# Kernel tuning notes

Measured on AMD Instinct MI355X. Metric: run time of the kernel, lower is better.

Reference implementation:

```python
import jax, jax.numpy as jnp
import numpy as np
import math

T, N, D, H = 1024, 8, 1024, 16
HD = D // H  # head_dim = 64


def setup_inputs() -> dict:
    key = jax.random.key(0)
    k1, k2, k3, k4 = jax.random.split(key, 4)
    scale = 1.0 / math.sqrt(D)  # roughly xavier-scale params
    return {
        "x": jax.random.normal(k1, (T, N, D), dtype=jnp.float32),
        "q_weight": jax.random.normal(k2, (D, H, HD), dtype=jnp.float32) * scale,
        "v_weight": jax.random.normal(k3, (D, H, HD), dtype=jnp.float32) * scale,
        "out_w": jax.random.normal(k4, (D, D), dtype=jnp.float32) * scale,
        "out_b": jnp.zeros((D,), dtype=jnp.float32),
    }


def reference(x, q_weight, v_weight, out_w, out_b):
    inv_sqrt_hd = 1.0 / math.sqrt(HD)
    # q = k : (T, N, H, HD)
    q = jnp.einsum('tbm,mhd->tbhd', x, q_weight)
    q_sq = jnp.einsum('tbhd,tbhd->tbh', q, q)  # squared norms
    # squared L2 distance logits: (T, S, N, H)
    squared_dist = q_sq[:, None] + q_sq[None, :] - 2.0 * jnp.einsum('tbhd,sbhd->tsbh', q, q)
    attn_logits = -squared_dist * inv_sqrt_hd
    attn_weights = jax.nn.softmax(attn_logits, axis=1)  # softmax over source dim S
    # A = W_q W_q^T per head: (H, D, D)
    A = jnp.einsum('mhd,nhd->hmn', q_weight, q_weight) * inv_sqrt_hd
    XA = jnp.einsum('tbm,hmn->tbhn', x, A)           # (T, N, H, D)
    PXA = jnp.einsum('tsbh,sbhm->tbhm', attn_weights, XA)  # (T, N, H, D)
    PXAV = jnp.einsum('tbhm,mhd->tbhd', PXA, v_weight).reshape(T, N, D)
    return PXAV @ out_w.T + out_b
```

## Files before the change

kernel.cpp:

```cpp
#include <hip/hip_runtime.h>
#include <hip/hip_bf16.h>

#define T_ 1024
#define N_ 8
#define D_ 1024
#define H_ 16
#define HD_ 64

typedef __attribute__((ext_vector_type(8))) short bf16x8;
typedef __attribute__((ext_vector_type(4))) float f32x4;
typedef __attribute__((ext_vector_type(16))) float f32x16;
typedef __attribute__((ext_vector_type(4))) int i32x4;
typedef __attribute__((ext_vector_type(2))) int i32x2;
typedef unsigned short u16;
typedef unsigned int u32;

__device__ __forceinline__ float bf2f(u16 u){
  union { float f; unsigned int i; } v; v.i = ((unsigned int)u) << 16; return v.f;
}
__device__ __forceinline__ u16 f2bf(float f){
  union { float f; unsigned int i; } v; v.f = f;
  unsigned int r = v.i + 0x7FFFu + ((v.i >> 16) & 1u);
  return (u16)(r >> 16);
}
__device__ __forceinline__ u16 f2bf_fast(float f){
  __hip_bfloat16 h = __float2bfloat16(f);
  return *reinterpret_cast<u16*>(&h);
}
__device__ __forceinline__ float exp2_raw(float x){
  float r;
  asm("v_exp_f32 %0, %1" : "=v"(r) : "v"(x));
  return r;
}
__device__ __forceinline__ void gl_lds16(const u16* g, u16* l){
  __builtin_amdgcn_global_load_lds(
      (const __attribute__((address_space(1))) unsigned int*)g,
      (__attribute__((address_space(3))) unsigned int*)(unsigned int)(unsigned long long)l,
      16, 0, 0);
}

__global__ __launch_bounds__(256) void k_wqt(const float* __restrict__ Wq, u16* __restrict__ Wqt){
  __shared__ float tld[64][65];
  int m0 = blockIdx.x * 64, n0 = blockIdx.y * 64;
  int col = threadIdx.x & 63, rq = threadIdx.x >> 6;
  #pragma unroll
  for (int p = 0; p < 16; ++p){
    int row = rq * 16 + p;
    tld[row][col] = Wq[(size_t)(m0 + row) * D_ + n0 + col];
  }
  __syncthreads();
  #pragma unroll
  for (int p = 0; p < 16; ++p){
    int row = rq * 16 + p;
    Wqt[(size_t)(n0 + row) * D_ + m0 + col] = f2bf(tld[col][row]);
  }
}

__global__ __launch_bounds__(256) void k_bmatp(const float* __restrict__ qw, const float* __restrict__ vw,
                                               float* __restrict__ Bp){
  int h = (int)blockIdx.x >> 3, sp = (int)blockIdx.x & 7;
  int tid = threadIdx.x, lane = tid & 63, w = tid >> 6;
  int g = lane >> 4, c = lane & 15;
  __shared__ u16 Qt[64 * 72];
  __shared__ u16 Vt[64 * 72];
  f32x4 zero = {0.f, 0.f, 0.f, 0.f};
  f32x4 acc[4];
  #pragma unroll
  for (int eb = 0; eb < 4; ++eb) acc[eb] = zero;
  int m = tid >> 2, cg = tid & 3;
  for (int mt = sp * 128; mt < sp * 128 + 128; mt += 64){
    __syncthreads();
    #pragma unroll
    for (int q = 0; q < 4; ++q){
      int e0 = cg * 16 + q * 4;
      f32x4 vq = *(const f32x4*)(qw + (size_t)(mt + m) * D_ + h * 64 + e0);
      f32x4 vv = *(const f32x4*)(vw + (size_t)(mt + m) * D_ + h * 64 + e0);
      #pragma unroll
      for (int j = 0; j < 4; ++j){
        Qt[(e0 + j) * 72 + m] = f2bf_fast(vq[j]);
        Vt[(e0 + j) * 72 + m] = f2bf_fast(vv[j]);
      }
    }
    __syncthreads();
    #pragma unroll
    for (int kk = 0; kk < 2; ++kk){
      bf16x8 av = *(const bf16x8*)&Vt[(w * 16 + c) * 72 + kk * 32 + g * 8];
      #pragma unroll
      for (int eb = 0; eb < 4; ++eb){
        bf16x8 bq = *(const bf16x8*)&Qt[(eb * 16 + c) * 72 + kk * 32 + g * 8];
        acc[eb] = __builtin_amdgcn_mfma_f32_16x16x32_bf16(av, bq, acc[eb], 0, 0, 0);
      }
    }
  }
  #pragma unroll
  for (int eb = 0; eb < 4; ++eb)
    #pragma unroll
    for (int r = 0; r < 4; ++r){
      int d = w * 16 + g * 4 + r, e = eb * 16 + c;
      Bp[(((size_t)sp * 16 + h) * 64 + d) * 64 + e] = acc[eb][r];
    }
}

__global__ __launch_bounds__(256) void k_bred(const float* __restrict__ Bp, u16* __restrict__ Bt){
  int i = blockIdx.x * 256 + threadIdx.x;
  float s = 0.f;
  #pragma unroll
  for (int j = 0; j < 8; ++j) s += Bp[(size_t)j * 65536 + i];
  Bt[i] = f2bf(s * 0.125f);
}

__device__ __forceinline__ int swz(int row, int colbyte){
  return row * 64 + (((colbyte) ^ ((row & 7) << 4)) >> 1);
}

template<int A_F32, int B_F32, int EPI>
__global__ __launch_bounds__(256) void k_gemm(const void* __restrict__ A_, const void* __restrict__ B_,
                                              void* __restrict__ Cv, const float* __restrict__ bias,
                                              int M, int N, int K){
  int nbn = N >> 7;
  int ii = (int)blockIdx.x;
  int sw = (ii & 7) * 64 + (ii >> 3);
  int bm = sw / nbn, bn = sw % nbn;
  int tid = threadIdx.x, lane = tid & 63, wid = tid >> 6;
  int wr = wid >> 1, wc = wid & 1, g = lane >> 4, c = lane & 15;
  __shared__ u16 As[128 * 64];
  __shared__ u16 Bs[128 * 64];
  f32x4 zero = {0.f, 0.f, 0.f, 0.f};
  f32x4 acc[4][4];
  #pragma unroll
  for (int m = 0; m < 4; ++m)
    #pragma unroll
    for (int n = 0; n < 4; ++n) acc[m][n] = zero;
  for (int kt = 0; kt < K; kt += 64){
    __syncthreads();
    #pragma unroll
    for (int p = 0; p < 4; ++p){
      int ci = tid + p * 256;
      int row = ci >> 3, c8 = ci & 7;
      int dst = swz(row, c8 * 16);
      if (A_F32){
        const float* A = (const float*)A_;
        const float* src = A + (size_t)(bm * 128 + row) * K + kt + c8 * 8;
        f32x4 v0 = *(const f32x4*)src;
        f32x4 v1 = *(const f32x4*)(src + 4);
        union { u16 u[8]; i32x4 v; } pk;
        #pragma unroll
        for (int j = 0; j < 4; ++j){ pk.u[j] = f2bf_fast(v0[j]); pk.u[4 + j] = f2bf_fast(v1[j]); }
        *(i32x4*)&As[dst] = pk.v;
      } else {
        const u16* A = (const u16*)A_;
        *(i32x4*)&As[dst] = *(const i32x4*)(A + (size_t)(bm * 128 + row) * K + kt + c8 * 8);
      }
      if (B_F32){
        const float* B = (const float*)B_;
        const float* src = B + (size_t)(bn * 128 + row) * K + kt + c8 * 8;
        f32x4 v0 = *(const f32x4*)src;
        f32x4 v1 = *(const f32x4*)(src + 4);
        union { u16 u[8]; i32x4 v; } pk;
        #pragma unroll
        for (int j = 0; j < 4; ++j){ pk.u[j] = f2bf_fast(v0[j]); pk.u[4 + j] = f2bf_fast(v1[j]); }
        *(i32x4*)&Bs[dst] = pk.v;
      } else {
        const u16* B = (const u16*)B_;
        *(i32x4*)&Bs[dst] = *(const i32x4*)(B + (size_t)(bn * 128 + row) * K + kt + c8 * 8);
      }
    }
    __syncthreads();
    #pragma unroll
    for (int kk = 0; kk < 2; ++kk){
      bf16x8 af[4], bfr[4];
      #pragma unroll
      for (int m = 0; m < 4; ++m){
        int row = wr * 64 + m * 16 + c;
        af[m] = *(const bf16x8*)&As[swz(row, kk * 64 + g * 16)];
      }
      #pragma unroll
      for (int n = 0; n < 4; ++n){
        int row = wc * 64 + n * 16 + c;
        bfr[n] = *(const bf16x8*)&Bs[swz(row, kk * 64 + g * 16)];
      }
      #pragma unroll
      for (int m = 0; m < 4; ++m)
        #pragma unroll
        for (int n = 0; n < 4; ++n)
          acc[m][n] = __builtin_amdgcn_mfma_f32_16x16x32_bf16(af[m], bfr[n], acc[m][n], 0, 0, 0);
    }
  }
  #pragma unroll
  for (int m = 0; m < 4; ++m)
    #pragma unroll
    for (int n = 0; n < 4; ++n)
      #pragma unroll
      for (int r = 0; r < 4; ++r){
        int row = bm * 128 + wr * 64 + m * 16 + g * 4 + r;
        int col = bn * 128 + wc * 64 + n * 16 + c;
        float v = acc[m][n][r];
        if (EPI == 0){
          int t = row >> 3, b = row & 7, hh = col >> 6, dd = col & 63;
          ((u16*)Cv)[(((size_t)(b * H_ + hh)) * T_ + t) * HD_ + dd] = f2bf(v);
        } else {
          ((float*)Cv)[(size_t)row * N + col] = v + bias[col];
        }
      }
}

__global__ __launch_bounds__(64) void k_u(const u16* __restrict__ qb, const u16* __restrict__ Bt,
                                          u16* __restrict__ ubt, float* __restrict__ qsq){
  int bh = blockIdx.x >> 4, tt = blockIdx.x & 15;
  int h = bh & 15, t0 = tt * 64;
  int lane = threadIdx.x, g = lane >> 4, c = lane & 15;
  const float QS_SCALE = 0.125f * 1.44269504088896340736f;
  bf16x8 af[4][2], bq[4][2];
  #pragma unroll
  for (int mf = 0; mf < 4; ++mf)
    #pragma unroll
    for (int kk = 0; kk < 2; ++kk)
      af[mf][kk] = *(const bf16x8*)(Bt + ((size_t)(h * 64 + mf * 16 + c)) * 64 + kk * 32 + g * 8);
  #pragma unroll
  for (int nf = 0; nf < 4; ++nf)
    #pragma unroll
    for (int kk = 0; kk < 2; ++kk)
      bq[nf][kk] = *(const bf16x8*)(qb + ((size_t)(bh * 1024 + t0 + nf * 16 + c)) * 64 + kk * 32 + g * 8);
  #pragma unroll
  for (int nf = 0; nf < 4; ++nf){
    float ss = 0.f;
    #pragma unroll
    for (int kk = 0; kk < 2; ++kk)
      #pragma unroll
      for (int j = 0; j < 8; ++j){ float f = bf2f((u16)bq[nf][kk][j]); ss = fmaf(f, f, ss); }
    ss += __shfl_xor(ss, 16);
    ss += __shfl_xor(ss, 32);
    if (lane < 16) qsq[(size_t)bh * 1024 + t0 + nf * 16 + lane] = ss * QS_SCALE;
  }
  f32x4 zero = {0.f, 0.f, 0.f, 0.f};
  f32x4 acc[4][4];
  #pragma unroll
  for (int mf = 0; mf < 4; ++mf)
    #pragma unroll
    for (int nf = 0; nf < 4; ++nf) acc[mf][nf] = zero;
  #pragma unroll
  for (int kk = 0; kk < 2; ++kk)
    #pragma unroll
    for (int mf = 0; mf < 4; ++mf)
      #pragma unroll
      for (int nf = 0; nf < 4; ++nf)
        acc[mf][nf] = __builtin_amdgcn_mfma_f32_16x16x32_bf16(af[mf][kk], bq[nf][kk], acc[mf][nf], 0, 0, 0);
  #pragma unroll
  for (int mf = 0; mf < 4; ++mf)
    #pragma unroll
    for (int nf = 0; nf < 4; ++nf)
      #pragma unroll
      for (int r = 0; r < 4; ++r)
        ubt[((size_t)(bh * 64 + mf * 16 + g * 4 + r)) * 1024 + t0 + nf * 16 + c] = f2bf(acc[mf][nf][r]);
}

__global__ __launch_bounds__(256, 4) void k_attn(const u16* __restrict__ qb, const u16* __restrict__ ubt,
                                                 const float* __restrict__ qsq, u16* __restrict__ obm){
  int i = (int)blockIdx.x;
  int bh = ((i & 7) << 4) + (i >> 6);
  int tt = (i >> 3) & 7;
  int b = bh >> 4, h = bh & 15;
  int tid = threadIdx.x, w = tid >> 6, lane = tid & 63;
  int lo = lane & 31, hi = lane >> 5;
  __shared__ u16 Kl[2][64 * 64];
  __shared__ u16 Ul[2][64 * 64];
  __shared__ float Qs[1024];
  const float C1 = 0.25f * 1.44269504088896340736f;
  int t0 = tt * 128 + w * 32;
  const u16* qbh = qb + (size_t)bh * 65536;
  const u16* ubh = ubt + (size_t)bh * 65536;
  const float* qsb = qsq + (size_t)bh * 1024;
  *(f32x4*)&Qs[tid * 4] = *(const f32x4*)(qsb + tid * 4);
  bf16x8 qB[4];
  #pragma unroll
  for (int kd = 0; kd < 4; ++kd)
    qB[kd] = *(const bf16x8*)(qbh + (t0 + lo) * 64 + kd * 16 + hi * 8);
  f32x16 o0 = {0,0,0,0,0,0,0,0,0,0,0,0,0,0,0,0};
  f32x16 o1 = {0,0,0,0,0,0,0,0,0,0,0,0,0,0,0,0};
  const f32x16 zero16 = {0,0,0,0,0,0,0,0,0,0,0,0,0,0,0,0};
  float l_c = 0.f;
  int slot0 = (w * 2 + 0) * 64 + lane, slot1 = (w * 2 + 1) * 64 + lane;
  int r0 = slot0 >> 3, sc0 = ((slot0 & 7) ^ (r0 & 7)) * 8;
  int r1 = slot1 >> 3, sc1 = ((slot1 & 7) ^ (r1 & 7)) * 8;
  int d0 = (w * 2 + 0) * 512, d1 = (w * 2 + 1) * 512;
  gl_lds16(qbh + r0 * 64 + sc0, &Kl[0][d0]);
  gl_lds16(qbh + r1 * 64 + sc1, &Kl[0][d1]);
  gl_lds16(ubh + (size_t)r0 * 1024 + sc0, &Ul[0][d0]);
  gl_lds16(ubh + (size_t)r1 * 1024 + sc1, &Ul[0][d1]);
  int cur = 0;
  for (int st = 0; st < 16; ++st){
    int s0 = st * 64;
    __syncthreads();
    if (st < 15){
      int s1 = s0 + 64;
      int nb = cur ^ 1;
      gl_lds16(qbh + (s1 + r0) * 64 + sc0, &Kl[nb][d0]);
      gl_lds16(qbh + (s1 + r1) * 64 + sc1, &Kl[nb][d1]);
      gl_lds16(ubh + (size_t)r0 * 1024 + s1 + sc0, &Ul[nb][d0]);
      gl_lds16(ubh + (size_t)r1 * 1024 + s1 + sc1, &Ul[nb][d1]);
    }
    const u16* Kc = &Kl[cur][0];
    const u16* Uc = &Ul[cur][0];
    #pragma unroll
    for (int ts = 0; ts < 2; ++ts){
      f32x16 sf = zero16;
      __builtin_amdgcn_s_setprio(1);
      #pragma unroll
      for (int kd = 0; kd < 4; ++kd){
        bf16x8 kA = *(const bf16x8*)&Kc[swz(ts * 32 + lo, kd * 32 + hi * 16)];
        sf = __builtin_amdgcn_mfma_f32_32x32x16_bf16(kA, qB[kd], sf, 0, 0, 0);
      }
      __builtin_amdgcn_s_setprio(0);
      f32x4 qs_[4];
      #pragma unroll
      for (int q = 0; q < 4; ++q)
        qs_[q] = *(const f32x4*)&Qs[s0 + ts * 32 + q * 8 + hi * 4];
      float p[16];
      #pragma unroll
      for (int r = 0; r < 16; ++r)
        p[r] = exp2_raw(fmaf(sf[r], C1, -qs_[r >> 2][r & 3]));
      float sA = ((p[0] + p[1]) + (p[2] + p[3])) + ((p[4] + p[5]) + (p[6] + p[7]));
      float sB = ((p[8] + p[9]) + (p[10] + p[11])) + ((p[12] + p[13]) + (p[14] + p[15]));
      l_c += sA + sB;
      u32 W[8];
      #pragma unroll
      for (int q = 0; q < 8; ++q)
        W[q] = ((u32)f2bf_fast(p[2 * q + 1]) << 16) | (u32)f2bf_fast(p[2 * q]);
      #pragma unroll
      for (int ml = 0; ml < 2; ++ml){
        int m_g = ts * 2 + ml;
        int base = ml * 4;
        i32x2 sw0 = __builtin_amdgcn_permlane32_swap((int)W[base + 0], (int)W[base + 2], false, false);
        i32x2 sw1 = __builtin_amdgcn_permlane32_swap((int)W[base + 1], (int)W[base + 3], false, false);
        union { u32 wd[4]; bf16x8 v; } pa;
        pa.wd[0] = (u32)sw0[0]; pa.wd[1] = (u32)sw1[0]; pa.wd[2] = (u32)sw0[1]; pa.wd[3] = (u32)sw1[1];
        bf16x8 u0 = *(const bf16x8*)&Uc[swz(lo, m_g * 32 + hi * 16)];
        bf16x8 u1 = *(const bf16x8*)&Uc[swz(32 + lo, m_g * 32 + hi * 16)];
        __builtin_amdgcn_s_setprio(1);
        o0 = __builtin_amdgcn_mfma_f32_32x32x16_bf16(pa.v, u0, o0, 0, 0, 0);
        o1 = __builtin_amdgcn_mfma_f32_32x32x16_bf16(pa.v, u1, o1, 0, 0, 0);
        __builtin_amdgcn_s_setprio(0);
      }
    }
    cur ^= 1;
  }
  l_c += __shfl_xor(l_c, 32);
  float inv = 1.0f / l_c;
  #pragma unroll
  for (int r = 0; r < 16; ++r){
    int tr = (r & 3) + 8 * (r >> 2) + 4 * hi;
    float invr = __shfl(inv, tr);
    size_t rowb = ((size_t)((t0 + tr) * 8 + b)) * 1024 + h * 64;
    obm[rowb + lo] = f2bf(o0[r] * invr);
    obm[rowb + 32 + lo] = f2bf(o1[r] * invr);
  }
}

extern "C" void kernel_launch(void* const* d_in, const int* in_sizes, int n_in,
                              void* d_out, int out_size, void* d_ws, size_t ws_size,
                              hipStream_t stream) {
  const float* x   = (const float*)d_in[0];
  const float* qw  = (const float*)d_in[1];
  const float* vw  = (const float*)d_in[2];
  const float* ow  = (const float*)d_in[3];
  const float* ob_bias = (const float*)d_in[4];
  float* out = (float*)d_out;

  float* Bp = (float*)d_out;
  u16* qb  = (u16*)d_out;
  u16* ubt = (u16*)((char*)d_out + (size_t)16 * 1024 * 1024);

  char* ws = (char*)d_ws;
  size_t off = 0;
  auto alloc = [&](size_t bytes) -> void* {
    void* p = ws + off;
    off += (bytes + 255) & ~(size_t)255;
    return p;
  };
  u16*   wqt = (u16*)  alloc((size_t)1024 * 1024 * 2);
  u16*   obm = (u16*)  alloc((size_t)8192 * 1024 * 2);
  float* qsq = (float*)alloc((size_t)128 * 1024 * 4);
  u16*   Bt  = (u16*)  alloc((size_t)16 * 64 * 64 * 2);

  k_bmatp<<<128, 256, 0, stream>>>(qw, vw, Bp);
  k_bred<<<256, 256, 0, stream>>>(Bp, Bt);
  k_wqt<<<dim3(16, 16), 256, 0, stream>>>(qw, wqt);
  k_gemm<1, 0, 0><<<512, 256, 0, stream>>>(x, wqt, qb, nullptr, 8192, 1024, 1024);
  k_u<<<2048, 64, 0, stream>>>(qb, Bt, ubt, qsq);
  k_attn<<<1024, 256, 0, stream>>>(qb, ubt, qsq, obm);
  k_gemm<0, 1, 1><<<512, 256, 0, stream>>>(obm, ow, out, ob_bias, 8192, 1024, 1024);
}
```

Measured before the change: 136.1 us.

## Software-pipeline attention loop: PV MFMA of previous tile overlaps current QK and softmax

```diff
diff --git a/kernel.cpp b/kernel.cpp
--- a/kernel.cpp
+++ b/kernel.cpp
@@ -263,14 +263,12 @@
   int tid = threadIdx.x, w = tid >> 6, lane = tid & 63;
   int lo = lane & 31, hi = lane >> 5;
   __shared__ u16 Kl[2][64 * 64];
-  __shared__ u16 Ul[2][64 * 64];
-  __shared__ float Qs[1024];
+  __shared__ u16 Ul[3][64 * 64];
   const float C1 = 0.25f * 1.44269504088896340736f;
   int t0 = tt * 128 + w * 32;
   const u16* qbh = qb + (size_t)bh * 65536;
   const u16* ubh = ubt + (size_t)bh * 65536;
   const float* qsb = qsq + (size_t)bh * 1024;
-  *(f32x4*)&Qs[tid * 4] = *(const f32x4*)(qsb + tid * 4);
   bf16x8 qB[4];
   #pragma unroll
   for (int kd = 0; kd < 4; ++kd)
@@ -279,6 +277,7 @@
   f32x16 o1 = {0,0,0,0,0,0,0,0,0,0,0,0,0,0,0,0};
   const f32x16 zero16 = {0,0,0,0,0,0,0,0,0,0,0,0,0,0,0,0};
   float l_c = 0.f;
+  u32 W[16];
   int slot0 = (w * 2 + 0) * 64 + lane, slot1 = (w * 2 + 1) * 64 + lane;
   int r0 = slot0 >> 3, sc0 = ((slot0 & 7) ^ (r0 & 7)) * 8;
   int r1 = slot1 >> 3, sc1 = ((slot1 & 7) ^ (r1 & 7)) * 8;
@@ -287,62 +286,98 @@
   gl_lds16(qbh + r1 * 64 + sc1, &Kl[0][d1]);
   gl_lds16(ubh + (size_t)r0 * 1024 + sc0, &Ul[0][d0]);
   gl_lds16(ubh + (size_t)r1 * 1024 + sc1, &Ul[0][d1]);
-  int cur = 0;
+  __syncthreads();
+  int ub = 0, pub = 0;
   for (int st = 0; st < 16; ++st){
     int s0 = st * 64;
-    __syncthreads();
+    int kb = st & 1;
     if (st < 15){
       int s1 = s0 + 64;
-      int nb = cur ^ 1;
-      gl_lds16(qbh + (s1 + r0) * 64 + sc0, &Kl[nb][d0]);
-      gl_lds16(qbh + (s1 + r1) * 64 + sc1, &Kl[nb][d1]);
-      gl_lds16(ubh + (size_t)r0 * 1024 + s1 + sc0, &Ul[nb][d0]);
-      gl_lds16(ubh + (size_t)r1 * 1024 + s1 + sc1, &Ul[nb][d1]);
-    }
-    const u16* Kc = &Kl[cur][0];
-    const u16* Uc = &Ul[cur][0];
-    #pragma unroll
-    for (int ts = 0; ts < 2; ++ts){
-      f32x16 sf = zero16;
+      int nub = (ub == 2) ? 0 : ub + 1;
+      gl_lds16(qbh + (s1 + r0) * 64 + sc0, &Kl[kb ^ 1][d0]);
+      gl_lds16(qbh + (s1 + r1) * 64 + sc1, &Kl[kb ^ 1][d1]);
+      gl_lds16(ubh + (size_t)r0 * 1024 + s1 + sc0, &Ul[nub][d0]);
+      gl_lds16(ubh + (size_t)r1 * 1024 + s1 + sc1, &Ul[nub][d1]);
+    }
+    if (st > 0){
+      const u16* Up = &Ul[pub][0];
       __builtin_amdgcn_s_setprio(1);
       #pragma unroll
-      for (int kd = 0; kd < 4; ++kd){
-        bf16x8 kA = *(const bf16x8*)&Kc[swz(ts * 32 + lo, kd * 32 + hi * 16)];
-        sf = __builtin_amdgcn_mfma_f32_32x32x16_bf16(kA, qB[kd], sf, 0, 0, 0);
-      }
-      __builtin_amdgcn_s_setprio(0);
-      f32x4 qs_[4];
-      #pragma unroll
-      for (int q = 0; q < 4; ++q)
-        qs_[q] = *(const f32x4*)&Qs[s0 + ts * 32 + q * 8 + hi * 4];
-      float p[16];
-      #pragma unroll
-      for (int r = 0; r < 16; ++r)
-        p[r] = exp2_raw(fmaf(sf[r], C1, -qs_[r >> 2][r & 3]));
-      float sA = ((p[0] + p[1]) + (p[2] + p[3])) + ((p[4] + p[5]) + (p[6] + p[7]));
-      float sB = ((p[8] + p[9]) + (p[10] + p[11])) + ((p[12] + p[13]) + (p[14] + p[15]));
-      l_c += sA + sB;
-      u32 W[8];
-      #pragma unroll
-      for (int q = 0; q < 8; ++q)
-        W[q] = ((u32)f2bf_fast(p[2 * q + 1]) << 16) | (u32)f2bf_fast(p[2 * q]);
-      #pragma unroll
-      for (int ml = 0; ml < 2; ++ml){
-        int m_g = ts * 2 + ml;
-        int base = ml * 4;
+      for (int m_g = 0; m_g < 4; ++m_g){
+        int base = (m_g >> 1) * 8 + (m_g & 1) * 4;
         i32x2 sw0 = __builtin_amdgcn_permlane32_swap((int)W[base + 0], (int)W[base + 2], false, false);
         i32x2 sw1 = __builtin_amdgcn_permlane32_swap((int)W[base + 1], (int)W[base + 3], false, false);
         union { u32 wd[4]; bf16x8 v; } pa;
         pa.wd[0] = (u32)sw0[0]; pa.wd[1] = (u32)sw1[0]; pa.wd[2] = (u32)sw0[1]; pa.wd[3] = (u32)sw1[1];
-        bf16x8 u0 = *(const bf16x8*)&Uc[swz(lo, m_g * 32 + hi * 16)];
-        bf16x8 u1 = *(const bf16x8*)&Uc[swz(32 + lo, m_g * 32 + hi * 16)];
-        __builtin_amdgcn_s_setprio(1);
+        bf16x8 u0 = *(const bf16x8*)&Up[swz(lo, m_g * 32 + hi * 16)];
+        bf16x8 u1 = *(const bf16x8*)&Up[swz(32 + lo, m_g * 32 + hi * 16)];
         o0 = __builtin_amdgcn_mfma_f32_32x32x16_bf16(pa.v, u0, o0, 0, 0, 0);
         o1 = __builtin_amdgcn_mfma_f32_32x32x16_bf16(pa.v, u1, o1, 0, 0, 0);
-        __builtin_amdgcn_s_setprio(0);
-      }
-    }
-    cur ^= 1;
+      }
+      __builtin_amdgcn_s_setprio(0);
+    }
+    const u16* Kc = &Kl[kb][0];
+    f32x16 sfA = zero16, sfB = zero16;
+    __builtin_amdgcn_s_setprio(1);
+    #pragma unroll
+    for (int kd = 0; kd < 4; ++kd){
+      bf16x8 kA = *(const bf16x8*)&Kc[swz(lo, kd * 32 + hi * 16)];
+      sfA = __builtin_amdgcn_mfma_f32_32x32x16_bf16(kA, qB[kd], sfA, 0, 0, 0);
+    }
+    #pragma unroll
+    for (int kd = 0; kd < 4; ++kd){
+      bf16x8 kB = *(const bf16x8*)&Kc[swz(32 + lo, kd * 32 + hi * 16)];
+      sfB = __builtin_amdgcn_mfma_f32_32x32x16_bf16(kB, qB[kd], sfB, 0, 0, 0);
+    }
+    __builtin_amdgcn_s_setprio(0);
+    {
+      f32x4 qs_[4];
+      #pragma unroll
+      for (int q = 0; q < 4; ++q)
+        qs_[q] = *(const f32x4*)(qsb + s0 + q * 8 + hi * 4);
+      float p[16];
+      #pragma unroll
+      for (int r = 0; r < 16; ++r)
+        p[r] = exp2_raw(fmaf(sfA[r], C1, -qs_[r >> 2][r & 3]));
+      l_c += (((p[0] + p[1]) + (p[2] + p[3])) + ((p[4] + p[5]) + (p[6] + p[7])))
+           + (((p[8] + p[9]) + (p[10] + p[11])) + ((p[12] + p[13]) + (p[14] + p[15])));
+      #pragma unroll
+      for (int q = 0; q < 8; ++q)
+        W[q] = ((u32)f2bf_fast(p[2 * q + 1]) << 16) | (u32)f2bf_fast(p[2 * q]);
+    }
+    {
+      f32x4 qs_[4];
+      #pragma unroll
+      for (int q = 0; q < 4; ++q)
+        qs_[q] = *(const f32x4*)(qsb + s0 + 32 + q * 8 + hi * 4);
+      float p[16];
+      #pragma unroll
+      for (int r = 0; r < 16; ++r)
+        p[r] = exp2_raw(fmaf(sfB[r], C1, -qs_[r >> 2][r & 3]));
+      l_c += (((p[0] + p[1]) + (p[2] + p[3])) + ((p[4] + p[5]) + (p[6] + p[7])))
+           + (((p[8] + p[9]) + (p[10] + p[11])) + ((p[12] + p[13]) + (p[14] + p[15])));
+      #pragma unroll
+      for (int q = 0; q < 8; ++q)
+        W[8 + q] = ((u32)f2bf_fast(p[2 * q + 1]) << 16) | (u32)f2bf_fast(p[2 * q]);
+    }
+    __syncthreads();
+    pub = ub;
+    ub = (ub == 2) ? 0 : ub + 1;
+  }
+  {
+    const u16* Up = &Ul[pub][0];
+    #pragma unroll
+    for (int m_g = 0; m_g < 4; ++m_g){
+      int base = (m_g >> 1) * 8 + (m_g & 1) * 4;
+      i32x2 sw0 = __builtin_amdgcn_permlane32_swap((int)W[base + 0], (int)W[base + 2], false, false);
+      i32x2 sw1 = __builtin_amdgcn_permlane32_swap((int)W[base + 1], (int)W[base + 3], false, false);
+      union { u32 wd[4]; bf16x8 v; } pa;
+      pa.wd[0] = (u32)sw0[0]; pa.wd[1] = (u32)sw1[0]; pa.wd[2] = (u32)sw0[1]; pa.wd[3] = (u32)sw1[1];
+      bf16x8 u0 = *(const bf16x8*)&Up[swz(lo, m_g * 32 + hi * 16)];
+      bf16x8 u1 = *(const bf16x8*)&Up[swz(32 + lo, m_g * 32 + hi * 16)];
+      o0 = __builtin_amdgcn_mfma_f32_32x32x16_bf16(pa.v, u0, o0, 0, 0, 0);
+      o1 = __builtin_amdgcn_mfma_f32_32x32x16_bf16(pa.v, u1, o1, 0, 0, 0);
+    }
   }
   l_c += __shfl_xor(l_c, 32);
   float inv = 1.0f / l_c;
```

Result: slower. 151.7 us (+11.5%).
